# Kernel optimization log

Measured on AMD Instinct MI355X. Metric: run time of the kernel, lower is better.

The kernel has to match this reference:

```python
import jax, jax.numpy as jnp
import numpy as np

# Eigenvalue spec: (alpha, omega, multiplicity); field='complex' => d_state = sum(mul)
EIGS = [(-0.4, 0.0, 32), (-0.3, 3.14, 32), (-0.2, 6.28, 32), (-0.1, 12.57, 32),
        (-0.05, 25.13, 32), (-0.02, 50.27, 32), (-0.01, 100.53, 32), (-0.005, 201.06, 32)]
DELTA_MIN, DELTA_MAX = 1e-3, 1e-1
B_SZ, H, L = 8, 128, 8192  # batch, d_input, seq length


def setup_inputs() -> dict:
    key = jax.random.key(0)
    k_delta, k_bre, k_bim, k_cre, k_cim, k_d, k_u = jax.random.split(key, 7)
    # continuous-time diagonal state matrix Lambda (P,) complex
    Lam = np.concatenate([np.full(m, a + 1j * w, dtype=np.complex64) for a, w, m in EIGS])
    Lambda = jnp.asarray(Lam)  # (P,)
    P = Lambda.shape[0]
    # ZOH discretization (done at init in the torch module)
    Delta = DELTA_MIN + (DELTA_MAX - DELTA_MIN) * jax.random.uniform(k_delta, (P,), dtype=jnp.float32)
    Lambda_bar = jnp.exp(Lambda * Delta)  # (P,) complex64
    B = (jax.random.normal(k_bre, (P, H), dtype=jnp.float32)
         + 1j * jax.random.normal(k_bim, (P, H), dtype=jnp.float32))
    B_bar = (((Lambda_bar - 1.0) / Lambda)[:, None] * B).astype(jnp.complex64)  # (P,H)
    C_re = jax.random.normal(k_cre, (H, P), dtype=jnp.float32)
    C_im = jax.random.normal(k_cim, (H, P), dtype=jnp.float32)
    D = jax.random.normal(k_d, (H, H), dtype=jnp.float32)
    u = jax.random.normal(k_u, (B_SZ, H, L), dtype=jnp.float32)
    return {
        "u": u,
        "Lambda_bar_re": jnp.real(Lambda_bar), "Lambda_bar_im": jnp.imag(Lambda_bar),
        "B_bar_re": jnp.real(B_bar), "B_bar_im": jnp.imag(B_bar),
        "C_re": C_re, "C_im": C_im, "D": D,
    }


def reference(u, Lambda_bar_re, Lambda_bar_im, B_bar_re, B_bar_im, C_re, C_im, D):
    Lambda_bar = Lambda_bar_re + 1j * Lambda_bar_im          # (P,)
    B_bar = B_bar_re + 1j * B_bar_im                         # (P,H)
    C = C_re + 1j * C_im                                     # (H,P)
    uc = u.astype(B_bar.dtype)
    Bu = jnp.einsum('ph,bhl->bpl', B_bar, uc)                # (B,P,L) complex
    A = jnp.broadcast_to(Lambda_bar[None, :, None], Bu.shape)  # (B,P,L)
    # The repo's binary op computes the sequential recurrence x_t = A_t * (x_{t-1} + Bu_t).
    # Rewriting with Bu'_t = A_t * Bu_t gives x_t = A_t x_{t-1} + Bu'_t, which is the
    # standard (truly associative) first-order scan.
    ABu = A * Bu

    def binop(ei, ej):
        a_i, b_i = ei
        a_j, b_j = ej
        return a_j * a_i, a_j * b_i + b_j

    _, xs = jax.lax.associative_scan(binop, (A, ABu), axis=2)  # xs: (B,P,L)
    y = jnp.einsum('op,bpl->bol', C, xs).real + jnp.einsum('oh,bhl->bol', D, u)
    return jax.nn.gelu(y, approximate=False)  # torch nn.GELU default = exact erf
```

## Files before the change

kernel.cpp:

```cpp
#include <hip/hip_runtime.h>
#include <math.h>

#define Bn 8
#define Hd 128
#define Ld 8192
#define Pd 256
#define LC 32
#define NC 256

typedef __attribute__((ext_vector_type(8))) short bf16x8;
typedef __attribute__((ext_vector_type(4))) float f32x4;
#define MFMA16(a, b, c) __builtin_amdgcn_mfma_f32_16x16x32_bf16(a, b, c, 0, 0, 0)

__device__ __forceinline__ unsigned short f2bf(float f) {
  unsigned u = __float_as_uint(f);
  u = u + 0x7fffu + ((u >> 16) & 1u);
  return (unsigned short)(u >> 16);
}

#if __has_builtin(__builtin_amdgcn_cvt_pk_bf16_f32)
typedef __attribute__((ext_vector_type(2))) __bf16 v2bf_t;
__device__ __forceinline__ unsigned pack2(float a, float b) {
  v2bf_t r = __builtin_amdgcn_cvt_pk_bf16_f32(a, b);
  unsigned u;
  __builtin_memcpy(&u, &r, 4);
  return u;
}
#else
__device__ __forceinline__ unsigned pack2(float a, float b) {
  return (unsigned)f2bf(a) | ((unsigned)f2bf(b) << 16);
}
#endif

__device__ __forceinline__ float bflo(unsigned v) { return __uint_as_float(v << 16); }
__device__ __forceinline__ float bfhi(unsigned v) { return __uint_as_float(v & 0xffff0000u); }

__device__ __forceinline__ int xs_idx(int p, int j) {
  return j * 256 + ((((p >> 2) ^ (j & 7)) << 2) | (p & 3));
}

__global__ void k_prep(const float* __restrict__ Bre, const float* __restrict__ Bim,
                       const float* __restrict__ Cre, const float* __restrict__ Cim,
                       const float* __restrict__ Dm,
                       bf16x8* __restrict__ Bfr, bf16x8* __restrict__ Bfi,
                       bf16x8* __restrict__ Cf, bf16x8* __restrict__ Df) {
  int tid = blockIdx.x * 256 + threadIdx.x;
  int lane = tid & 63, slot = tid >> 6;
  int q = lane >> 4, ln = lane & 15;
  if (slot < 64) {
    int ks = slot >> 4, mt = slot & 15;
    int p = mt * 16 + ln;
    bf16x8 vr, vi;
#pragma unroll
    for (int e = 0; e < 8; ++e) {
      int h = ks * 32 + q * 8 + e;
      vr[e] = (short)f2bf(Bre[p * Hd + h]);
      vi[e] = (short)f2bf(Bim[p * Hd + h]);
    }
    Bfr[slot * 64 + lane] = vr;
    Bfi[slot * 64 + lane] = vi;
  } else if (slot < 64 + 128) {
    int s2 = slot - 64;
    int ks = s2 >> 3, mt = s2 & 7;
    int o = mt * 16 + ln;
    bf16x8 v;
#pragma unroll
    for (int e = 0; e < 8; ++e) {
      int kp = ks * 32 + q * 8 + e;
      int p = kp >> 1;
      float val = (kp & 1) ? -Cim[o * Pd + p] : Cre[o * Pd + p];
      v[e] = (short)f2bf(val);
    }
    Cf[s2 * 64 + lane] = v;
  } else if (slot < 64 + 128 + 32) {
    int s3 = slot - 192;
    int ks = s3 >> 3, mt = s3 & 7;
    int o = mt * 16 + ln;
    bf16x8 v;
#pragma unroll
    for (int e = 0; e < 8; ++e) {
      int h = ks * 32 + q * 8 + e;
      v[e] = (short)f2bf(Dm[o * Hd + h]);
    }
    Df[s3 * 64 + lane] = v;
  }
}

__device__ __forceinline__ void stage_u(const float* __restrict__ ub, unsigned* us32, int t) {
  int lane = t & 63, w = t >> 6;
  int j0 = 4 * (lane & 7);
  int h2 = 16 * w + 2 * (lane >> 3);
  const float* r0 = ub + (size_t)h2 * Ld + j0;
  float4 a0 = *(const float4*)r0;
  float4 a1 = *(const float4*)(r0 + Ld);
  const float* r2 = r0 + (size_t)64 * Ld;
  float4 b0 = *(const float4*)r2;
  float4 b1 = *(const float4*)(r2 + Ld);
  float ta0[4] = {a0.x, a0.y, a0.z, a0.w};
  float ta1[4] = {a1.x, a1.y, a1.z, a1.w};
  float tb0[4] = {b0.x, b0.y, b0.z, b0.w};
  float tb1[4] = {b1.x, b1.y, b1.z, b1.w};
#pragma unroll
  for (int i = 0; i < 4; ++i) {
    int j = j0 + i;
    int g1 = (h2 >> 3) ^ (j & 7);
    us32[(j * 256 + (g1 << 4) + ((2 * h2) & 15)) >> 2] = pack2(ta0[i], ta1[i]);
    int hb = h2 + 64;
    int g2 = (hb >> 3) ^ (j & 7);
    us32[(j * 256 + (g2 << 4) + ((2 * hb) & 15)) >> 2] = pack2(tb0[i], tb1[i]);
  }
}

__device__ __forceinline__ void compute_bu(const unsigned* us32,
                                           const bf16x8* __restrict__ Bfr,
                                           const bf16x8* __restrict__ Bfi,
                                           unsigned* xs32, int t) {
  int lane = t & 63, w = t >> 6, q = lane >> 4, ln = lane & 15;
  f32x4 zz = {0.f, 0.f, 0.f, 0.f};
  f32x4 aR[4][2], aI[4][2];
#pragma unroll
  for (int mt = 0; mt < 4; ++mt)
#pragma unroll
    for (int n = 0; n < 2; ++n) { aR[mt][n] = zz; aI[mt][n] = zz; }

#pragma unroll
  for (int ks = 0; ks < 4; ++ks) {
    bf16x8 ubf[2];
#pragma unroll
    for (int n = 0; n < 2; ++n) {
      int j = 16 * n + ln;
      int g = (4 * ks + q) ^ (j & 7);
      ubf[n] = *(const bf16x8*)((const char*)us32 + j * 256 + g * 16);
    }
#pragma unroll
    for (int mt = 0; mt < 4; ++mt) {
      int tI = ks * 16 + w * 4 + mt;
      bf16x8 ar = Bfr[tI * 64 + lane];
      bf16x8 ai = Bfi[tI * 64 + lane];
#pragma unroll
      for (int n = 0; n < 2; ++n) {
        aR[mt][n] = MFMA16(ar, ubf[n], aR[mt][n]);
        aI[mt][n] = MFMA16(ai, ubf[n], aI[mt][n]);
      }
    }
  }
#pragma unroll
  for (int mt = 0; mt < 4; ++mt)
#pragma unroll
    for (int n = 0; n < 2; ++n) {
      int p0 = w * 64 + mt * 16 + q * 4;
      int j = 16 * n + ln;
      int g = (p0 >> 2) ^ (j & 7);
      uint4 wv = make_uint4(pack2(aR[mt][n][0], aI[mt][n][0]),
                            pack2(aR[mt][n][1], aI[mt][n][1]),
                            pack2(aR[mt][n][2], aI[mt][n][2]),
                            pack2(aR[mt][n][3], aI[mt][n][3]));
      *(uint4*)(xs32 + j * 256 + g * 4) = wv;
    }
}

__global__ __launch_bounds__(256, 4) void k_chunk(
    const float* __restrict__ u, const float* __restrict__ lre,
    const float* __restrict__ lim, const bf16x8* __restrict__ Bfr,
    const bf16x8* __restrict__ Bfi, float2* __restrict__ E) {
  int bc = blockIdx.x;
  int b = bc >> 8, c = bc & 255;
  __shared__ __align__(16) unsigned char smem[8192 + 32768];
  unsigned* us32 = (unsigned*)smem;
  unsigned* xs32 = (unsigned*)(smem + 8192);
  int t = threadIdx.x;

  stage_u(u + (size_t)b * Hd * Ld + c * LC, us32, t);
  __syncthreads();
  compute_bu(us32, Bfr, Bfi, xs32, t);

  int p = t;
  float ax = lre[p], ay = lim[p];
  float xr = 0.f, xi = 0.f;
#pragma unroll
  for (int j = 0; j < LC; ++j) {
    unsigned v = xs32[xs_idx(p, j)];
    float sr = xr + bflo(v), si = xi + bfhi(v);
    xr = ax * sr - ay * si;
    xi = ax * si + ay * sr;
  }
  E[(size_t)bc * Pd + p] = make_float2(xr, xi);
}

__global__ __launch_bounds__(256) void k_scan(const float* __restrict__ lre,
                                              const float* __restrict__ lim,
                                              float2* __restrict__ E) {
  __shared__ float2 arr[32][8];
  int nb = blockIdx.x;
  int t = threadIdx.x;
  int pl = t & 7, rq = t >> 3;
  int b = nb >> 5;
  int p = ((nb & 31) << 3) + pl;
  float ax = lre[p], ay = lim[p];
  float mx = ax, my = ay;
#pragma unroll
  for (int k = 0; k < 5; ++k) {
    float nx = mx * mx - my * my, ny = 2.f * mx * my;
    mx = nx; my = ny;
  }
  size_t base = ((size_t)(b * NC + rq * 8)) * Pd + p;
  float2 pre[8];
  float cr = 0.f, ci = 0.f;
#pragma unroll
  for (int i = 0; i < 8; ++i) {
    float2 e = E[base + (size_t)i * Pd];
    pre[i] = make_float2(cr, ci);
    float nx = mx * cr - my * ci + e.x;
    float ny = mx * ci + my * cr + e.y;
    cr = nx; ci = ny;
  }
  float Mx = mx, My = my;
#pragma unroll
  for (int k = 0; k < 3; ++k) {
    float nx = Mx * Mx - My * My, ny = 2.f * Mx * My;
    Mx = nx; My = ny;
  }
  float Vx = cr, Vy = ci;
#pragma unroll
  for (int d = 1; d < 32; d <<= 1) {
    arr[rq][pl] = make_float2(Vx, Vy);
    __syncthreads();
    if (rq >= d) {
      float2 pv = arr[rq - d][pl];
      Vx += Mx * pv.x - My * pv.y;
      Vy += Mx * pv.y + My * pv.x;
    }
    __syncthreads();
    float nx = Mx * Mx - My * My, ny = 2.f * Mx * My;
    Mx = nx; My = ny;
  }
  arr[rq][pl] = make_float2(Vx, Vy);
  __syncthreads();
  float Cx = 0.f, Cy = 0.f;
  if (rq > 0) {
    float2 pv = arr[rq - 1][pl];
    Cx = pv.x; Cy = pv.y;
  }
  float tx = 1.f, ty = 0.f;
#pragma unroll
  for (int i = 0; i < 8; ++i) {
    float ox = pre[i].x + tx * Cx - ty * Cy;
    float oy = pre[i].y + tx * Cy + ty * Cx;
    E[base + (size_t)i * Pd] = make_float2(ox, oy);
    float nx = tx * mx - ty * my, ny = tx * my + ty * mx;
    tx = nx; ty = ny;
  }
}

__global__ __launch_bounds__(256, 4) void k_main(
    const float* __restrict__ u, const float* __restrict__ lre,
    const float* __restrict__ lim, const bf16x8* __restrict__ Bfr,
    const bf16x8* __restrict__ Bfi, const bf16x8* __restrict__ Cf,
    const bf16x8* __restrict__ Df, const float2* __restrict__ E,
    float* __restrict__ out) {
  int bc = blockIdx.x;
  int b = bc >> 8, c = bc & 255;
  __shared__ __align__(16) unsigned char smem[8192 + 32768];
  unsigned* us32 = (unsigned*)smem;
  unsigned* xs32 = (unsigned*)(smem + 8192);
  int t = threadIdx.x;
  int lane = t & 63, w = t >> 6, q = lane >> 4, ln = lane & 15;
  int p = t;

  float2 xin = E[(size_t)bc * Pd + p];
  float ax = lre[p], ay = lim[p];

  stage_u(u + (size_t)b * Hd * Ld + c * LC, us32, t);
  __syncthreads();
  compute_bu(us32, Bfr, Bfi, xs32, t);

  {
    float xr = xin.x, xi = xin.y;
#pragma unroll
    for (int j = 0; j < LC; ++j) {
      int idx = xs_idx(p, j);
      unsigned v = xs32[idx];
      float sr = xr + bflo(v), si = xi + bfhi(v);
      xr = ax * sr - ay * si;
      xi = ax * si + ay * sr;
      xs32[idx] = pack2(xr, xi);
    }
  }
  __syncthreads();

  f32x4 zz = {0.f, 0.f, 0.f, 0.f};
  f32x4 acc[2][2] = {{zz, zz}, {zz, zz}};
#pragma unroll
  for (int ks = 0; ks < 16; ++ks) {
    bf16x8 xb[2];
#pragma unroll
    for (int n = 0; n < 2; ++n) {
      int j = 16 * n + ln;
      int g = (4 * ks + q) ^ (j & 7);
      xb[n] = *(const bf16x8*)((const char*)xs32 + j * 1024 + g * 16);
    }
#pragma unroll
    for (int mt = 0; mt < 2; ++mt) {
      bf16x8 cf = Cf[(ks * 8 + w * 2 + mt) * 64 + lane];
#pragma unroll
      for (int n = 0; n < 2; ++n) acc[mt][n] = MFMA16(cf, xb[n], acc[mt][n]);
    }
  }
#pragma unroll
  for (int ks = 0; ks < 4; ++ks) {
    bf16x8 ubf[2];
#pragma unroll
    for (int n = 0; n < 2; ++n) {
      int j = 16 * n + ln;
      int g = (4 * ks + q) ^ (j & 7);
      ubf[n] = *(const bf16x8*)((const char*)us32 + j * 256 + g * 16);
    }
#pragma unroll
    for (int mt = 0; mt < 2; ++mt) {
      bf16x8 df = Df[(ks * 8 + w * 2 + mt) * 64 + lane];
#pragma unroll
      for (int n = 0; n < 2; ++n) acc[mt][n] = MFMA16(df, ubf[n], acc[mt][n]);
    }
  }

#pragma unroll
  for (int mt = 0; mt < 2; ++mt)
#pragma unroll
    for (int n = 0; n < 2; ++n)
#pragma unroll
      for (int r = 0; r < 4; ++r) {
        int o = w * 32 + mt * 16 + q * 4 + r;
        int l = c * LC + 16 * n + ln;
        float vy = acc[mt][n][r];
        float e2 = __builtin_amdgcn_exp2f(-2.4554670f * vy);
        float gy = vy * __builtin_amdgcn_rcpf(1.0f + e2);
        out[((size_t)(b * Hd + o)) * Ld + l] = gy;
      }
}

extern "C" void kernel_launch(void* const* d_in, const int* in_sizes, int n_in,
                              void* d_out, int out_size, void* d_ws, size_t ws_size,
                              hipStream_t stream) {
  const float* u   = (const float*)d_in[0];
  const float* lre = (const float*)d_in[1];
  const float* lim = (const float*)d_in[2];
  const float* Bre = (const float*)d_in[3];
  const float* Bim = (const float*)d_in[4];
  const float* Cre = (const float*)d_in[5];
  const float* Cim = (const float*)d_in[6];
  const float* Dm  = (const float*)d_in[7];
  float* out = (float*)d_out;

  char* ws = (char*)d_ws;
  bf16x8* Bfr = (bf16x8*)(ws);
  bf16x8* Bfi = (bf16x8*)(ws + 65536);
  bf16x8* Cf  = (bf16x8*)(ws + 131072);
  bf16x8* Df  = (bf16x8*)(ws + 262144);
  float2* E   = (float2*)(ws + (1 << 20));

  k_prep<<<56, 256, 0, stream>>>(Bre, Bim, Cre, Cim, Dm, Bfr, Bfi, Cf, Df);
  k_chunk<<<Bn * NC, 256, 0, stream>>>(u, lre, lim, Bfr, Bfi, E);
  k_scan<<<256, 256, 0, stream>>>(lre, lim, E);
  k_main<<<Bn * NC, 256, 0, stream>>>(u, lre, lim, Bfr, Bfi, Cf, Df, E, out);
}
```

Before: 145.3 us.

## Process each 32-step chunk in two 16-step halves to shrink LDS and registers

```diff
diff --git a/kernel.cpp b/kernel.cpp
--- a/kernel.cpp
+++ b/kernel.cpp
@@ -6,6 +6,7 @@
 #define Ld 8192
 #define Pd 256
 #define LC 32
+#define LH 16
 #define NC 256
 
 typedef __attribute__((ext_vector_type(8))) short bf16x8;
@@ -86,103 +87,78 @@
   }
 }
 
-__device__ __forceinline__ void stage_u(const float* __restrict__ ub, unsigned* us32, int t) {
-  int lane = t & 63, w = t >> 6;
-  int j0 = 4 * (lane & 7);
-  int h2 = 16 * w + 2 * (lane >> 3);
+__device__ __forceinline__ void stage_u16(const float* __restrict__ ub,
+                                          unsigned* us32, int t) {
+  int h2 = (t >> 2) * 2;
+  int j0 = (t & 3) * 4;
   const float* r0 = ub + (size_t)h2 * Ld + j0;
   float4 a0 = *(const float4*)r0;
   float4 a1 = *(const float4*)(r0 + Ld);
-  const float* r2 = r0 + (size_t)64 * Ld;
-  float4 b0 = *(const float4*)r2;
-  float4 b1 = *(const float4*)(r2 + Ld);
   float ta0[4] = {a0.x, a0.y, a0.z, a0.w};
   float ta1[4] = {a1.x, a1.y, a1.z, a1.w};
-  float tb0[4] = {b0.x, b0.y, b0.z, b0.w};
-  float tb1[4] = {b1.x, b1.y, b1.z, b1.w};
 #pragma unroll
   for (int i = 0; i < 4; ++i) {
     int j = j0 + i;
-    int g1 = (h2 >> 3) ^ (j & 7);
-    us32[(j * 256 + (g1 << 4) + ((2 * h2) & 15)) >> 2] = pack2(ta0[i], ta1[i]);
-    int hb = h2 + 64;
-    int g2 = (hb >> 3) ^ (j & 7);
-    us32[(j * 256 + (g2 << 4) + ((2 * hb) & 15)) >> 2] = pack2(tb0[i], tb1[i]);
-  }
-}
-
-__device__ __forceinline__ void compute_bu(const unsigned* us32,
-                                           const bf16x8* __restrict__ Bfr,
-                                           const bf16x8* __restrict__ Bfi,
-                                           unsigned* xs32, int t) {
+    int g = (h2 >> 3) ^ (j & 7);
+    us32[(j * 256 + (g << 4) + ((2 * h2) & 15)) >> 2] = pack2(ta0[i], ta1[i]);
+  }
+}
+
+__device__ __forceinline__ void compute_bu16(const unsigned* us32,
+                                             const bf16x8* __restrict__ Bfr,
+                                             const bf16x8* __restrict__ Bfi,
+                                             unsigned* xs32, int t) {
   int lane = t & 63, w = t >> 6, q = lane >> 4, ln = lane & 15;
   f32x4 zz = {0.f, 0.f, 0.f, 0.f};
-  f32x4 aR[4][2], aI[4][2];
-#pragma unroll
-  for (int mt = 0; mt < 4; ++mt)
-#pragma unroll
-    for (int n = 0; n < 2; ++n) { aR[mt][n] = zz; aI[mt][n] = zz; }
-
+  f32x4 aR[4] = {zz, zz, zz, zz}, aI[4] = {zz, zz, zz, zz};
 #pragma unroll
   for (int ks = 0; ks < 4; ++ks) {
-    bf16x8 ubf[2];
-#pragma unroll
-    for (int n = 0; n < 2; ++n) {
-      int j = 16 * n + ln;
-      int g = (4 * ks + q) ^ (j & 7);
-      ubf[n] = *(const bf16x8*)((const char*)us32 + j * 256 + g * 16);
-    }
+    int g = (4 * ks + q) ^ (ln & 7);
+    bf16x8 ubf = *(const bf16x8*)((const char*)us32 + ln * 256 + g * 16);
 #pragma unroll
     for (int mt = 0; mt < 4; ++mt) {
       int tI = ks * 16 + w * 4 + mt;
-      bf16x8 ar = Bfr[tI * 64 + lane];
-      bf16x8 ai = Bfi[tI * 64 + lane];
-#pragma unroll
-      for (int n = 0; n < 2; ++n) {
-        aR[mt][n] = MFMA16(ar, ubf[n], aR[mt][n]);
-        aI[mt][n] = MFMA16(ai, ubf[n], aI[mt][n]);
-      }
-    }
-  }
-#pragma unroll
-  for (int mt = 0; mt < 4; ++mt)
-#pragma unroll
-    for (int n = 0; n < 2; ++n) {
-      int p0 = w * 64 + mt * 16 + q * 4;
-      int j = 16 * n + ln;
-      int g = (p0 >> 2) ^ (j & 7);
-      uint4 wv = make_uint4(pack2(aR[mt][n][0], aI[mt][n][0]),
-                            pack2(aR[mt][n][1], aI[mt][n][1]),
-                            pack2(aR[mt][n][2], aI[mt][n][2]),
-                            pack2(aR[mt][n][3], aI[mt][n][3]));
-      *(uint4*)(xs32 + j * 256 + g * 4) = wv;
-    }
-}
-
-__global__ __launch_bounds__(256, 4) void k_chunk(
+      aR[mt] = MFMA16(Bfr[tI * 64 + lane], ubf, aR[mt]);
+      aI[mt] = MFMA16(Bfi[tI * 64 + lane], ubf, aI[mt]);
+    }
+  }
+#pragma unroll
+  for (int mt = 0; mt < 4; ++mt) {
+    int p0 = w * 64 + mt * 16 + q * 4;
+    int g = (p0 >> 2) ^ (ln & 7);
+    uint4 wv = make_uint4(pack2(aR[mt][0], aI[mt][0]), pack2(aR[mt][1], aI[mt][1]),
+                          pack2(aR[mt][2], aI[mt][2]), pack2(aR[mt][3], aI[mt][3]));
+    *(uint4*)(xs32 + ln * 256 + g * 4) = wv;
+  }
+}
+
+__global__ __launch_bounds__(256, 6) void k_chunk(
     const float* __restrict__ u, const float* __restrict__ lre,
     const float* __restrict__ lim, const bf16x8* __restrict__ Bfr,
     const bf16x8* __restrict__ Bfi, float2* __restrict__ E) {
   int bc = blockIdx.x;
   int b = bc >> 8, c = bc & 255;
-  __shared__ __align__(16) unsigned char smem[8192 + 32768];
+  __shared__ __align__(16) unsigned char smem[4096 + 16384];
   unsigned* us32 = (unsigned*)smem;
-  unsigned* xs32 = (unsigned*)(smem + 8192);
+  unsigned* xs32 = (unsigned*)(smem + 4096);
   int t = threadIdx.x;
-
-  stage_u(u + (size_t)b * Hd * Ld + c * LC, us32, t);
-  __syncthreads();
-  compute_bu(us32, Bfr, Bfi, xs32, t);
-
   int p = t;
   float ax = lre[p], ay = lim[p];
+  const float* ub = u + (size_t)b * Hd * Ld + c * LC;
   float xr = 0.f, xi = 0.f;
 #pragma unroll
-  for (int j = 0; j < LC; ++j) {
-    unsigned v = xs32[xs_idx(p, j)];
-    float sr = xr + bflo(v), si = xi + bfhi(v);
-    xr = ax * sr - ay * si;
-    xi = ax * si + ay * sr;
+  for (int hf = 0; hf < 2; ++hf) {
+    if (hf) __syncthreads();
+    stage_u16(ub + hf * LH, us32, t);
+    __syncthreads();
+    compute_bu16(us32, Bfr, Bfi, xs32, t);
+#pragma unroll
+    for (int j = 0; j < LH; ++j) {
+      unsigned v = xs32[xs_idx(p, j)];
+      float sr = xr + bflo(v), si = xi + bfhi(v);
+      xr = ax * sr - ay * si;
+      xi = ax * si + ay * sr;
+    }
   }
   E[(size_t)bc * Pd + p] = make_float2(xr, xi);
 }
@@ -252,7 +228,7 @@
   }
 }
 
-__global__ __launch_bounds__(256, 4) void k_main(
+__global__ __launch_bounds__(256, 6) void k_main(
     const float* __restrict__ u, const float* __restrict__ lre,
     const float* __restrict__ lim, const bf16x8* __restrict__ Bfr,
     const bf16x8* __restrict__ Bfi, const bf16x8* __restrict__ Cf,
@@ -260,24 +236,26 @@
     float* __restrict__ out) {
   int bc = blockIdx.x;
   int b = bc >> 8, c = bc & 255;
-  __shared__ __align__(16) unsigned char smem[8192 + 32768];
+  __shared__ __align__(16) unsigned char smem[4096 + 16384];
   unsigned* us32 = (unsigned*)smem;
-  unsigned* xs32 = (unsigned*)(smem + 8192);
+  unsigned* xs32 = (unsigned*)(smem + 4096);
   int t = threadIdx.x;
   int lane = t & 63, w = t >> 6, q = lane >> 4, ln = lane & 15;
   int p = t;
 
   float2 xin = E[(size_t)bc * Pd + p];
   float ax = lre[p], ay = lim[p];
-
-  stage_u(u + (size_t)b * Hd * Ld + c * LC, us32, t);
-  __syncthreads();
-  compute_bu(us32, Bfr, Bfi, xs32, t);
-
-  {
-    float xr = xin.x, xi = xin.y;
-#pragma unroll
-    for (int j = 0; j < LC; ++j) {
+  const float* ub = u + (size_t)b * Hd * Ld + c * LC;
+  float xr = xin.x, xi = xin.y;
+
+#pragma unroll
+  for (int hf = 0; hf < 2; ++hf) {
+    if (hf) __syncthreads();
+    stage_u16(ub + hf * LH, us32, t);
+    __syncthreads();
+    compute_bu16(us32, Bfr, Bfi, xs32, t);
+#pragma unroll
+    for (int j = 0; j < LH; ++j) {
       int idx = xs_idx(p, j);
       unsigned v = xs32[idx];
       float sr = xr + bflo(v), si = xi + bfhi(v);
@@ -285,57 +263,39 @@
       xi = ax * si + ay * sr;
       xs32[idx] = pack2(xr, xi);
     }
-  }
-  __syncthreads();
-
-  f32x4 zz = {0.f, 0.f, 0.f, 0.f};
-  f32x4 acc[2][2] = {{zz, zz}, {zz, zz}};
-#pragma unroll
-  for (int ks = 0; ks < 16; ++ks) {
-    bf16x8 xb[2];
-#pragma unroll
-    for (int n = 0; n < 2; ++n) {
-      int j = 16 * n + ln;
-      int g = (4 * ks + q) ^ (j & 7);
-      xb[n] = *(const bf16x8*)((const char*)xs32 + j * 1024 + g * 16);
-    }
-#pragma unroll
-    for (int mt = 0; mt < 2; ++mt) {
-      bf16x8 cf = Cf[(ks * 8 + w * 2 + mt) * 64 + lane];
-#pragma unroll
-      for (int n = 0; n < 2; ++n) acc[mt][n] = MFMA16(cf, xb[n], acc[mt][n]);
-    }
-  }
-#pragma unroll
-  for (int ks = 0; ks < 4; ++ks) {
-    bf16x8 ubf[2];
-#pragma unroll
-    for (int n = 0; n < 2; ++n) {
-      int j = 16 * n + ln;
-      int g = (4 * ks + q) ^ (j & 7);
-      ubf[n] = *(const bf16x8*)((const char*)us32 + j * 256 + g * 16);
-    }
-#pragma unroll
-    for (int mt = 0; mt < 2; ++mt) {
-      bf16x8 df = Df[(ks * 8 + w * 2 + mt) * 64 + lane];
-#pragma unroll
-      for (int n = 0; n < 2; ++n) acc[mt][n] = MFMA16(df, ubf[n], acc[mt][n]);
-    }
-  }
-
-#pragma unroll
-  for (int mt = 0; mt < 2; ++mt)
-#pragma unroll
-    for (int n = 0; n < 2; ++n)
+    __syncthreads();
+
+    f32x4 zz = {0.f, 0.f, 0.f, 0.f};
+    f32x4 acc[2] = {zz, zz};
+#pragma unroll
+    for (int ks = 0; ks < 16; ++ks) {
+      int g = (4 * ks + q) ^ (ln & 7);
+      bf16x8 xb = *(const bf16x8*)((const char*)xs32 + ln * 1024 + g * 16);
+#pragma unroll
+      for (int mt = 0; mt < 2; ++mt)
+        acc[mt] = MFMA16(Cf[(ks * 8 + w * 2 + mt) * 64 + lane], xb, acc[mt]);
+    }
+#pragma unroll
+    for (int ks = 0; ks < 4; ++ks) {
+      int g = (4 * ks + q) ^ (ln & 7);
+      bf16x8 ubf = *(const bf16x8*)((const char*)us32 + ln * 256 + g * 16);
+#pragma unroll
+      for (int mt = 0; mt < 2; ++mt)
+        acc[mt] = MFMA16(Df[(ks * 8 + w * 2 + mt) * 64 + lane], ubf, acc[mt]);
+    }
+
+    int l = c * LC + hf * LH + ln;
+#pragma unroll
+    for (int mt = 0; mt < 2; ++mt)
 #pragma unroll
       for (int r = 0; r < 4; ++r) {
         int o = w * 32 + mt * 16 + q * 4 + r;
-        int l = c * LC + 16 * n + ln;
-        float vy = acc[mt][n][r];
+        float vy = acc[mt][r];
         float e2 = __builtin_amdgcn_exp2f(-2.4554670f * vy);
         float gy = vy * __builtin_amdgcn_rcpf(1.0f + e2);
         out[((size_t)(b * Hd + o)) * Ld + l] = gy;
       }
+  }
 }
 
 extern "C" void kernel_launch(void* const* d_in, const int* in_sizes, int n_in,
```

Result: slower. 238.3 us (+64.0%).

## Split state dimension into two halves to halve Bu shared memory buffer

Applied to the files above, without the earlier changes.

```diff
diff --git a/kernel.cpp b/kernel.cpp
--- a/kernel.cpp
+++ b/kernel.cpp
@@ -35,8 +35,8 @@
 __device__ __forceinline__ float bflo(unsigned v) { return __uint_as_float(v << 16); }
 __device__ __forceinline__ float bfhi(unsigned v) { return __uint_as_float(v & 0xffff0000u); }
 
-__device__ __forceinline__ int xs_idx(int p, int j) {
-  return j * 256 + ((((p >> 2) ^ (j & 7)) << 2) | (p & 3));
+__device__ __forceinline__ int xsh_idx(int pt, int j) {
+  return j * 128 + ((((pt >> 2) ^ (j & 7)) << 2) | (pt & 3));
 }
 
 __global__ void k_prep(const float* __restrict__ Bre, const float* __restrict__ Bim,
@@ -111,15 +111,15 @@
   }
 }
 
-__device__ __forceinline__ void compute_bu(const unsigned* us32,
-                                           const bf16x8* __restrict__ Bfr,
-                                           const bf16x8* __restrict__ Bfi,
-                                           unsigned* xs32, int t) {
+__device__ __forceinline__ void compute_bu_half(const unsigned* us32,
+                                                const bf16x8* __restrict__ Bfr,
+                                                const bf16x8* __restrict__ Bfi,
+                                                unsigned* xs16, int t, int h) {
   int lane = t & 63, w = t >> 6, q = lane >> 4, ln = lane & 15;
   f32x4 zz = {0.f, 0.f, 0.f, 0.f};
-  f32x4 aR[4][2], aI[4][2];
-#pragma unroll
-  for (int mt = 0; mt < 4; ++mt)
+  f32x4 aR[2][2], aI[2][2];
+#pragma unroll
+  for (int mt = 0; mt < 2; ++mt)
 #pragma unroll
     for (int n = 0; n < 2; ++n) { aR[mt][n] = zz; aI[mt][n] = zz; }
 
@@ -133,8 +133,8 @@
       ubf[n] = *(const bf16x8*)((const char*)us32 + j * 256 + g * 16);
     }
 #pragma unroll
-    for (int mt = 0; mt < 4; ++mt) {
-      int tI = ks * 16 + w * 4 + mt;
+    for (int mt = 0; mt < 2; ++mt) {
+      int tI = ks * 16 + w * 4 + h * 2 + mt;
       bf16x8 ar = Bfr[tI * 64 + lane];
       bf16x8 ai = Bfi[tI * 64 + lane];
 #pragma unroll
@@ -145,44 +145,51 @@
     }
   }
 #pragma unroll
-  for (int mt = 0; mt < 4; ++mt)
+  for (int mt = 0; mt < 2; ++mt)
 #pragma unroll
     for (int n = 0; n < 2; ++n) {
-      int p0 = w * 64 + mt * 16 + q * 4;
+      int ptq = (w << 3) | (mt << 2) | q;
       int j = 16 * n + ln;
-      int g = (p0 >> 2) ^ (j & 7);
+      int g = ptq ^ (j & 7);
       uint4 wv = make_uint4(pack2(aR[mt][n][0], aI[mt][n][0]),
                             pack2(aR[mt][n][1], aI[mt][n][1]),
                             pack2(aR[mt][n][2], aI[mt][n][2]),
                             pack2(aR[mt][n][3], aI[mt][n][3]));
-      *(uint4*)(xs32 + j * 256 + g * 4) = wv;
-    }
-}
-
-__global__ __launch_bounds__(256, 4) void k_chunk(
+      *(uint4*)(xs16 + j * 128 + g * 4) = wv;
+    }
+}
+
+__global__ __launch_bounds__(256, 6) void k_chunk(
     const float* __restrict__ u, const float* __restrict__ lre,
     const float* __restrict__ lim, const bf16x8* __restrict__ Bfr,
     const bf16x8* __restrict__ Bfi, float2* __restrict__ E) {
   int bc = blockIdx.x;
   int b = bc >> 8, c = bc & 255;
-  __shared__ __align__(16) unsigned char smem[8192 + 32768];
+  __shared__ __align__(16) unsigned char smem[8192 + 16384];
   unsigned* us32 = (unsigned*)smem;
-  unsigned* xs32 = (unsigned*)(smem + 8192);
+  unsigned* xs16 = (unsigned*)(smem + 8192);
   int t = threadIdx.x;
+  int p = t;
+  int hme = (t >> 5) & 1;
+  int pt = ((t >> 6) << 5) | (t & 31);
+  float ax = lre[p], ay = lim[p];
 
   stage_u(u + (size_t)b * Hd * Ld + c * LC, us32, t);
   __syncthreads();
-  compute_bu(us32, Bfr, Bfi, xs32, t);
-
-  int p = t;
-  float ax = lre[p], ay = lim[p];
+
   float xr = 0.f, xi = 0.f;
 #pragma unroll
-  for (int j = 0; j < LC; ++j) {
-    unsigned v = xs32[xs_idx(p, j)];
-    float sr = xr + bflo(v), si = xi + bfhi(v);
-    xr = ax * sr - ay * si;
-    xi = ax * si + ay * sr;
+  for (int h = 0; h < 2; ++h) {
+    compute_bu_half(us32, Bfr, Bfi, xs16, t, h);
+    if (hme == h) {
+#pragma unroll
+      for (int j = 0; j < LC; ++j) {
+        unsigned v = xs16[xsh_idx(pt, j)];
+        float sr = xr + bflo(v), si = xi + bfhi(v);
+        xr = ax * sr - ay * si;
+        xi = ax * si + ay * sr;
+      }
+    }
   }
   E[(size_t)bc * Pd + p] = make_float2(xr, xi);
 }
@@ -260,52 +267,62 @@
     float* __restrict__ out) {
   int bc = blockIdx.x;
   int b = bc >> 8, c = bc & 255;
-  __shared__ __align__(16) unsigned char smem[8192 + 32768];
+  __shared__ __align__(16) unsigned char smem[8192 + 16384];
   unsigned* us32 = (unsigned*)smem;
-  unsigned* xs32 = (unsigned*)(smem + 8192);
+  unsigned* xs16 = (unsigned*)(smem + 8192);
   int t = threadIdx.x;
   int lane = t & 63, w = t >> 6, q = lane >> 4, ln = lane & 15;
   int p = t;
+  int hme = (t >> 5) & 1;
+  int pt = ((t >> 6) << 5) | (t & 31);
 
   float2 xin = E[(size_t)bc * Pd + p];
   float ax = lre[p], ay = lim[p];
 
   stage_u(u + (size_t)b * Hd * Ld + c * LC, us32, t);
   __syncthreads();
-  compute_bu(us32, Bfr, Bfi, xs32, t);
-
-  {
-    float xr = xin.x, xi = xin.y;
-#pragma unroll
-    for (int j = 0; j < LC; ++j) {
-      int idx = xs_idx(p, j);
-      unsigned v = xs32[idx];
-      float sr = xr + bflo(v), si = xi + bfhi(v);
-      xr = ax * sr - ay * si;
-      xi = ax * si + ay * sr;
-      xs32[idx] = pack2(xr, xi);
-    }
-  }
-  __syncthreads();
 
   f32x4 zz = {0.f, 0.f, 0.f, 0.f};
   f32x4 acc[2][2] = {{zz, zz}, {zz, zz}};
-#pragma unroll
-  for (int ks = 0; ks < 16; ++ks) {
-    bf16x8 xb[2];
-#pragma unroll
-    for (int n = 0; n < 2; ++n) {
-      int j = 16 * n + ln;
-      int g = (4 * ks + q) ^ (j & 7);
-      xb[n] = *(const bf16x8*)((const char*)xs32 + j * 1024 + g * 16);
-    }
-#pragma unroll
-    for (int mt = 0; mt < 2; ++mt) {
-      bf16x8 cf = Cf[(ks * 8 + w * 2 + mt) * 64 + lane];
-#pragma unroll
-      for (int n = 0; n < 2; ++n) acc[mt][n] = MFMA16(cf, xb[n], acc[mt][n]);
-    }
-  }
+  float xr = xin.x, xi = xin.y;
+
+#pragma unroll
+  for (int h = 0; h < 2; ++h) {
+    if (h) __syncthreads();
+    compute_bu_half(us32, Bfr, Bfi, xs16, t, h);
+    if (hme == h) {
+#pragma unroll
+      for (int j = 0; j < LC; ++j) {
+        int idx = xsh_idx(pt, j);
+        unsigned v = xs16[idx];
+        float sr = xr + bflo(v), si = xi + bfhi(v);
+        xr = ax * sr - ay * si;
+        xi = ax * si + ay * sr;
+        xs16[idx] = pack2(xr, xi);
+      }
+    }
+    __syncthreads();
+
+#pragma unroll
+    for (int ksl = 0; ksl < 8; ++ksl) {
+      int ks = ((ksl >> 1) << 2) | (h << 1) | (ksl & 1);
+      int gb = ((ks >> 2) << 3) | ((ks & 1) << 2) | q;
+      bf16x8 xb[2];
+#pragma unroll
+      for (int n = 0; n < 2; ++n) {
+        int j = 16 * n + ln;
+        int g = gb ^ (j & 7);
+        xb[n] = *(const bf16x8*)((const char*)xs16 + j * 512 + g * 16);
+      }
+#pragma unroll
+      for (int mt = 0; mt < 2; ++mt) {
+        bf16x8 cf = Cf[(ks * 8 + w * 2 + mt) * 64 + lane];
+#pragma unroll
+        for (int n = 0; n < 2; ++n) acc[mt][n] = MFMA16(cf, xb[n], acc[mt][n]);
+      }
+    }
+  }
+
 #pragma unroll
   for (int ks = 0; ks < 4; ++ks) {
     bf16x8 ubf[2];
```

New measurement: 183.2 us. 1.26x slower.

## Split output into zero-state chunk partial and carry-state correction pass

Applied to the files above, without the earlier changes.

```diff
diff --git a/kernel.cpp b/kernel.cpp
--- a/kernel.cpp
+++ b/kernel.cpp
@@ -159,32 +159,83 @@
     }
 }
 
-__global__ __launch_bounds__(256, 4) void k_chunk(
+__global__ __launch_bounds__(256, 4) void k_chunkP(
     const float* __restrict__ u, const float* __restrict__ lre,
     const float* __restrict__ lim, const bf16x8* __restrict__ Bfr,
-    const bf16x8* __restrict__ Bfi, float2* __restrict__ E) {
+    const bf16x8* __restrict__ Bfi, const bf16x8* __restrict__ Cf,
+    const bf16x8* __restrict__ Df, float2* __restrict__ E,
+    uint4* __restrict__ P0v) {
   int bc = blockIdx.x;
   int b = bc >> 8, c = bc & 255;
   __shared__ __align__(16) unsigned char smem[8192 + 32768];
   unsigned* us32 = (unsigned*)smem;
   unsigned* xs32 = (unsigned*)(smem + 8192);
   int t = threadIdx.x;
+  int lane = t & 63, w = t >> 6, q = lane >> 4, ln = lane & 15;
+  int p = t;
+  float ax = lre[p], ay = lim[p];
 
   stage_u(u + (size_t)b * Hd * Ld + c * LC, us32, t);
   __syncthreads();
   compute_bu(us32, Bfr, Bfi, xs32, t);
 
-  int p = t;
-  float ax = lre[p], ay = lim[p];
-  float xr = 0.f, xi = 0.f;
-#pragma unroll
-  for (int j = 0; j < LC; ++j) {
-    unsigned v = xs32[xs_idx(p, j)];
-    float sr = xr + bflo(v), si = xi + bfhi(v);
-    xr = ax * sr - ay * si;
-    xi = ax * si + ay * sr;
-  }
-  E[(size_t)bc * Pd + p] = make_float2(xr, xi);
+  {
+    float xr = 0.f, xi = 0.f;
+#pragma unroll
+    for (int j = 0; j < LC; ++j) {
+      int idx = xs_idx(p, j);
+      unsigned v = xs32[idx];
+      float sr = xr + bflo(v), si = xi + bfhi(v);
+      xr = ax * sr - ay * si;
+      xi = ax * si + ay * sr;
+      xs32[idx] = pack2(xr, xi);
+    }
+    E[(size_t)bc * Pd + p] = make_float2(xr, xi);
+  }
+  __syncthreads();
+
+  f32x4 zz = {0.f, 0.f, 0.f, 0.f};
+  f32x4 acc[2][2] = {{zz, zz}, {zz, zz}};
+#pragma unroll
+  for (int ks = 0; ks < 16; ++ks) {
+    bf16x8 xb[2];
+#pragma unroll
+    for (int n = 0; n < 2; ++n) {
+      int j = 16 * n + ln;
+      int g = (4 * ks + q) ^ (j & 7);
+      xb[n] = *(const bf16x8*)((const char*)xs32 + j * 1024 + g * 16);
+    }
+#pragma unroll
+    for (int mt = 0; mt < 2; ++mt) {
+      bf16x8 cf = Cf[(ks * 8 + w * 2 + mt) * 64 + lane];
+#pragma unroll
+      for (int n = 0; n < 2; ++n) acc[mt][n] = MFMA16(cf, xb[n], acc[mt][n]);
+    }
+  }
+#pragma unroll
+  for (int ks = 0; ks < 4; ++ks) {
+    bf16x8 ubf[2];
+#pragma unroll
+    for (int n = 0; n < 2; ++n) {
+      int j = 16 * n + ln;
+      int g = (4 * ks + q) ^ (j & 7);
+      ubf[n] = *(const bf16x8*)((const char*)us32 + j * 256 + g * 16);
+    }
+#pragma unroll
+    for (int mt = 0; mt < 2; ++mt) {
+      bf16x8 df = Df[(ks * 8 + w * 2 + mt) * 64 + lane];
+#pragma unroll
+      for (int n = 0; n < 2; ++n) acc[mt][n] = MFMA16(df, ubf[n], acc[mt][n]);
+    }
+  }
+
+  uint4* dst = P0v + (size_t)bc * 512 + t * 2;
+#pragma unroll
+  for (int mt = 0; mt < 2; ++mt)
+    dst[mt] = make_uint4(pack2(acc[mt][0][0], acc[mt][1][0]),
+                         pack2(acc[mt][0][1], acc[mt][1][1]),
+                         pack2(acc[mt][0][2], acc[mt][1][2]),
+                         pack2(acc[mt][0][3], acc[mt][1][3]));
 }
 
 __global__ __launch_bounds__(256) void k_scan(const float* __restrict__ lre,
@@ -252,39 +303,30 @@
   }
 }
 
-__global__ __launch_bounds__(256, 4) void k_main(
-    const float* __restrict__ u, const float* __restrict__ lre,
-    const float* __restrict__ lim, const bf16x8* __restrict__ Bfr,
-    const bf16x8* __restrict__ Bfi, const bf16x8* __restrict__ Cf,
-    const bf16x8* __restrict__ Df, const float2* __restrict__ E,
-    float* __restrict__ out) {
+__global__ __launch_bounds__(256, 4) void k_main2(
+    const float* __restrict__ lre, const float* __restrict__ lim,
+    const bf16x8* __restrict__ Cf, const float2* __restrict__ E,
+    const uint4* __restrict__ P0v, float* __restrict__ out) {
   int bc = blockIdx.x;
   int b = bc >> 8, c = bc & 255;
-  __shared__ __align__(16) unsigned char smem[8192 + 32768];
-  unsigned* us32 = (unsigned*)smem;
-  unsigned* xs32 = (unsigned*)(smem + 8192);
+  __shared__ __align__(16) unsigned xs32[LC * 256];
   int t = threadIdx.x;
   int lane = t & 63, w = t >> 6, q = lane >> 4, ln = lane & 15;
   int p = t;
 
+  const uint4* src = P0v + (size_t)bc * 512 + t * 2;
+  uint4 pA = src[0];
+  uint4 pB = src[1];
   float2 xin = E[(size_t)bc * Pd + p];
   float ax = lre[p], ay = lim[p];
 
-  stage_u(u + (size_t)b * Hd * Ld + c * LC, us32, t);
-  __syncthreads();
-  compute_bu(us32, Bfr, Bfi, xs32, t);
-
-  {
-    float xr = xin.x, xi = xin.y;
-#pragma unroll
-    for (int j = 0; j < LC; ++j) {
-      int idx = xs_idx(p, j);
-      unsigned v = xs32[idx];
-      float sr = xr + bflo(v), si = xi + bfhi(v);
-      xr = ax * sr - ay * si;
-      xi = ax * si + ay * sr;
-      xs32[idx] = pack2(xr, xi);
-    }
+  float gr = ax * xin.x - ay * xin.y;
+  float gi = ax * xin.y + ay * xin.x;
+#pragma unroll
+  for (int j = 0; j < LC; ++j) {
+    xs32[xs_idx(p, j)] = pack2(gr, gi);
+    float nr = ax * gr - ay * gi, ni = ax * gi + ay * gr;
+    gr = nr; gi = ni;
   }
   __syncthreads();
 
@@ -306,23 +348,8 @@
       for (int n = 0; n < 2; ++n) acc[mt][n] = MFMA16(cf, xb[n], acc[mt][n]);
     }
   }
-#pragma unroll
-  for (int ks = 0; ks < 4; ++ks) {
-    bf16x8 ubf[2];
-#pragma unroll
-    for (int n = 0; n < 2; ++n) {
-      int j = 16 * n + ln;
-      int g = (4 * ks + q) ^ (j & 7);
-      ubf[n] = *(const bf16x8*)((const char*)us32 + j * 256 + g * 16);
-    }
-#pragma unroll
-    for (int mt = 0; mt < 2; ++mt) {
-      bf16x8 df = Df[(ks * 8 + w * 2 + mt) * 64 + lane];
-#pragma unroll
-      for (int n = 0; n < 2; ++n) acc[mt][n] = MFMA16(df, ubf[n], acc[mt][n]);
-    }
-  }
-
+
+  unsigned pw[2][4] = {{pA.x, pA.y, pA.z, pA.w}, {pB.x, pB.y, pB.z, pB.w}};
 #pragma unroll
   for (int mt = 0; mt < 2; ++mt)
 #pragma unroll
@@ -331,7 +358,8 @@
       for (int r = 0; r < 4; ++r) {
         int o = w * 32 + mt * 16 + q * 4 + r;
         int l = c * LC + 16 * n + ln;
-        float vy = acc[mt][n][r];
+        float pv = n ? bfhi(pw[mt][r]) : bflo(pw[mt][r]);
+        float vy = acc[mt][n][r] + pv;
         float e2 = __builtin_amdgcn_exp2f(-2.4554670f * vy);
         float gy = vy * __builtin_amdgcn_rcpf(1.0f + e2);
         out[((size_t)(b * Hd + o)) * Ld + l] = gy;
@@ -356,10 +384,11 @@
   bf16x8* Bfi = (bf16x8*)(ws + 65536);
   bf16x8* Cf  = (bf16x8*)(ws + 131072);
   bf16x8* Df  = (bf16x8*)(ws + 262144);
-  float2* E   = (float2*)(ws + (1 << 20));
+  float2* E   = (float2*)(ws + (1u << 20));
+  uint4*  P0  = (uint4*)(ws + (16u << 20));
 
   k_prep<<<56, 256, 0, stream>>>(Bre, Bim, Cre, Cim, Dm, Bfr, Bfi, Cf, Df);
-  k_chunk<<<Bn * NC, 256, 0, stream>>>(u, lre, lim, Bfr, Bfi, E);
+  k_chunkP<<<Bn * NC, 256, 0, stream>>>(u, lre, lim, Bfr, Bfi, Cf, Df, E, P0);
   k_scan<<<256, 256, 0, stream>>>(lre, lim, E);
-  k_main<<<Bn * NC, 256, 0, stream>>>(u, lre, lim, Bfr, Bfi, Cf, Df, E, out);
-}
+  k_main2<<<Bn * NC, 256, 0, stream>>>(lre, lim, Cf, E, P0, out);
+}
```

Result: no change. 147.4 us (+1.4%).
